# Kernel optimization log

Measured on AMD Instinct MI355X. Metric: run time of the kernel, lower is better.

## Reference

```python
import jax, jax.numpy as jnp
import numpy as np

N_NODES = 170000
N_EDGES = 1200000
IN_C, HID_C, OUT_C = 128, 128, 40
BN_EPS = 1e-5


def setup_inputs() -> dict:
    key = jax.random.key(0)
    ks = jax.random.split(key, 12)
    def glorot(k, fan_in, fan_out):
        lim = (6.0 / (fan_in + fan_out)) ** 0.5
        return jax.random.uniform(k, (fan_in, fan_out), jnp.float32, -lim, lim)
    x = jax.random.normal(ks[0], (N_NODES, IN_C), jnp.float32)
    edge_index = jax.random.randint(ks[1], (2, N_EDGES), 0, N_NODES, jnp.int64)
    return {
        "x": x,
        "edge_index": edge_index,
        "W0": glorot(ks[2], IN_C, HID_C), "b0": jnp.zeros((HID_C,), jnp.float32),
        "g0": jnp.ones((HID_C,), jnp.float32), "be0": jnp.zeros((HID_C,), jnp.float32),
        "W1": glorot(ks[3], HID_C, HID_C), "b1": jnp.zeros((HID_C,), jnp.float32),
        "g1": jnp.ones((HID_C,), jnp.float32), "be1": jnp.zeros((HID_C,), jnp.float32),
        "W2": glorot(ks[4], HID_C, OUT_C), "b2": jnp.zeros((OUT_C,), jnp.float32),
    }


def _gcn_norm(edge_index, num_nodes):
    # add self-loops, symmetric normalization (PyG GCNConv default)
    loop = jnp.arange(num_nodes, dtype=edge_index.dtype)
    src = jnp.concatenate([edge_index[0], loop])
    dst = jnp.concatenate([edge_index[1], loop])
    deg = jax.ops.segment_sum(jnp.ones_like(dst, jnp.float32), dst, num_segments=num_nodes)
    dinv = jnp.where(deg > 0, jax.lax.rsqrt(deg), 0.0)
    norm = dinv[src] * dinv[dst]  # [E+N]
    return src, dst, norm


def _conv(h, W, b, src, dst, norm, num_nodes):
    h = h @ W                              # [N, out]
    msg = h[src] * norm[:, None]           # gather + scale, [E+N, out]
    out = jax.ops.segment_sum(msg, dst, num_segments=num_nodes)
    return out + b


def _bn_relu(h, g, be):
    mean = jnp.mean(h, axis=0)
    var = jnp.mean(jnp.square(h - mean), axis=0)  # biased, as torch BN training
    h = (h - mean) * jax.lax.rsqrt(var + BN_EPS) * g + be
    return jax.nn.relu(h)


def reference(x, edge_index, W0, b0, g0, be0, W1, b1, g1, be1, W2, b2):
    N = x.shape[0]
    src, dst, norm = _gcn_norm(edge_index, N)
    h = _bn_relu(_conv(x, W0, b0, src, dst, norm, N), g0, be0)
    h = _bn_relu(_conv(h, W1, b1, src, dst, norm, N), g1, be1)
    return _conv(h, W2, b2, src, dst, norm, N)
```

## Files before the change

kernel.cpp:

```cpp
#include <hip/hip_runtime.h>

#define BN_EPS 1e-5f
#define CAP 3072

using bf16x8 = __attribute__((ext_vector_type(8))) short;
using f32x4  = __attribute__((ext_vector_type(4))) float;

__device__ __forceinline__ unsigned int f2bf(float f) {
    unsigned int u = __float_as_uint(f);
    u += 0x7fffu + ((u >> 16) & 1u);
    return u >> 16;
}
__device__ __forceinline__ unsigned int f2bf2(float lo, float hi) {
    unsigned int r;
    asm("v_cvt_pk_bf16_f32 %0, %1, %2" : "=v"(r) : "v"(lo), "v"(hi));
    return r;
}
__device__ __forceinline__ float bflo(unsigned int u) { return __uint_as_float(u << 16); }
__device__ __forceinline__ float bfhi(unsigned int u) { return __uint_as_float(u & 0xffff0000u); }

__global__ __launch_bounds__(256) void k_bscatter(const int* __restrict__ ei,
                                                  int* __restrict__ bcur,
                                                  unsigned int* __restrict__ ebuf,
                                                  int E, int NB) {
    __shared__ int h[768];
    __shared__ int wb[768];
    for (int i = threadIdx.x; i < 768; i += 256) h[i] = 0;
    __syncthreads();
    int base = blockIdx.x * 8192;
    int rk[32];
    #pragma unroll
    for (int it = 0; it < 32; ++it) {
        int e = base + it * 256 + threadIdx.x;
        rk[it] = (e < E) ? atomicAdd(&h[ei[E + e] >> 8], 1) : 0;
    }
    __syncthreads();
    for (int i = threadIdx.x; i < NB; i += 256) {
        int c = h[i];
        wb[i] = c ? atomicAdd(&bcur[i], c) : 0;
    }
    __syncthreads();
    #pragma unroll
    for (int it = 0; it < 32; ++it) {
        int e = base + it * 256 + threadIdx.x;
        if (e < E) {
            unsigned s = (unsigned)ei[e], d = (unsigned)ei[E + e];
            int bk = (int)(d >> 8);
            int pos = wb[bk] + rk[it];
            if (pos < (bk + 1) * CAP)
                ebuf[pos] = s | ((d & 255u) << 24);
        }
    }
}

__global__ __launch_bounds__(256) void k_bfinal(const unsigned int* __restrict__ ebuf,
                                                const int* __restrict__ bcur,
                                                int* __restrict__ csr,
                                                int* __restrict__ rs,
                                                int* __restrict__ re,
                                                float* __restrict__ dinv, int N) {
    __shared__ int cnt[256];
    __shared__ int scn[256];
    __shared__ int cur[256];
    const int t = threadIdx.x, b = blockIdx.x;
    const int beg = b * CAP;
    const int cntE = min(bcur[b] - beg, CAP);
    cnt[t] = 0;
    __syncthreads();
    for (int j = t; j < cntE; j += 256)
        atomicAdd(&cnt[ebuf[beg + j] >> 24], 1);
    __syncthreads();
    int v = cnt[t];
    scn[t] = v;
    __syncthreads();
    for (int off = 1; off < 256; off <<= 1) {
        int x = (t >= off) ? scn[t - off] : 0;
        __syncthreads();
        scn[t] += x;
        __syncthreads();
    }
    int excl = scn[t] - v;
    int node = b * 256 + t;
    if (node < N) {
        rs[node]   = beg + excl;
        re[node]   = beg + excl + v;
        dinv[node] = rsqrtf((float)(1 + v));
    }
    cur[t] = beg + excl;
    __syncthreads();
    for (int j = t; j < cntE; j += 256) {
        unsigned e = ebuf[beg + j];
        int pos = atomicAdd(&cur[e >> 24], 1);
        csr[pos] = (int)(e & 0x00FFFFFFu);
    }
}

__global__ __launch_bounds__(256) void k_prepW3(const float* __restrict__ W0,
                                                const float* __restrict__ W1,
                                                const float* __restrict__ W2,
                                                unsigned short* __restrict__ Wf,
                                                int* __restrict__ bcur,
                                                float* __restrict__ stats, int NB) {
    int t = blockIdx.x * 256 + threadIdx.x;
    if (t < NB) bcur[t] = t * CAP;
    if (t < 512) stats[t] = 0.f;
    int wid = t >> 11;
    int f = t & 2047;
    const float* W = (wid == 0) ? W0 : (wid == 1) ? W1 : W2;
    int C = (wid == 2) ? 40 : 128;
    int lane = f & 63, frag = f >> 6;
    int kt = frag & 3, ct = frag >> 2;
    int r = lane & 15, q = lane >> 4;
    int col = ct * 16 + r;
    int kbase = kt * 32 + q * 8;
    unsigned int v[8];
    #pragma unroll
    for (int j = 0; j < 8; ++j)
        v[j] = (col < C) ? f2bf(W[(size_t)(kbase + j) * C + col]) : 0u;
    uint4 o;
    o.x = v[0] | (v[1] << 16);
    o.y = v[2] | (v[3] << 16);
    o.z = v[4] | (v[5] << 16);
    o.w = v[6] | (v[7] << 16);
    ((uint4*)Wf)[t] = o;
}

template <int NOCT, int OST>
__global__ __launch_bounds__(256) void k_gemm_mfma(
        const void* __restrict__ X, int xf32, const unsigned short* __restrict__ Wf,
        unsigned short* __restrict__ H, int N,
        const float* __restrict__ stats, const float* __restrict__ g,
        const float* __restrict__ be) {
    __shared__ unsigned short bF[NOCT * 4 * 512];
    __shared__ float2 bnss[128];
    const int tid = threadIdx.x;
    const int rowbase = blockIdx.x * 64;

    if (stats && tid < 128) {
        const float invN = 1.0f / (float)N;
        float mean = stats[tid] * invN;
        float var  = fmaf(-mean, mean, stats[128 + tid] * invN);
        float sc   = g[tid] * rsqrtf(var + BN_EPS);
        bnss[tid]  = make_float2(sc, fmaf(-mean, sc, be[tid]));
    }
    {
        const uint4* src = (const uint4*)Wf;
        uint4* dst = (uint4*)bF;
        #pragma unroll
        for (int i = 0; i < NOCT; ++i) dst[tid + 256 * i] = src[tid + 256 * i];
    }
    __syncthreads();

    const int wave = tid >> 6, lane = tid & 63;
    const int r = lane & 15, q = lane >> 4;
    const int row  = rowbase + wave * 16 + r;
    const int rowc = min(row, N - 1);

    bf16x8 afr[4];
    #pragma unroll
    for (int kt = 0; kt < 4; ++kt) {
        const int kc = kt * 32 + q * 8;
        float vv[8];
        if (xf32) {
            const float4* xp = (const float4*)((const float*)X + (size_t)rowc * 128 + kc);
            float4 p0 = xp[0], p1 = xp[1];
            vv[0] = p0.x; vv[1] = p0.y; vv[2] = p0.z; vv[3] = p0.w;
            vv[4] = p1.x; vv[5] = p1.y; vv[6] = p1.z; vv[7] = p1.w;
        } else {
            uint4 p = *((const uint4*)((const unsigned short*)X + (size_t)rowc * 128 + kc));
            vv[0] = bflo(p.x); vv[1] = bfhi(p.x);
            vv[2] = bflo(p.y); vv[3] = bfhi(p.y);
            vv[4] = bflo(p.z); vv[5] = bfhi(p.z);
            vv[6] = bflo(p.w); vv[7] = bfhi(p.w);
        }
        if (stats) {
            #pragma unroll
            for (int j = 0; j < 8; ++j) {
                float2 ss = bnss[kc + j];
                vv[j] = fmaxf(fmaf(vv[j], ss.x, ss.y), 0.0f);
            }
        }
        union { unsigned int u[4]; bf16x8 v; } pk;
        pk.u[0] = f2bf2(vv[0], vv[1]);
        pk.u[1] = f2bf2(vv[2], vv[3]);
        pk.u[2] = f2bf2(vv[4], vv[5]);
        pk.u[3] = f2bf2(vv[6], vv[7]);
        afr[kt] = pk.v;
    }

    f32x4 acc[NOCT];
    #pragma unroll
    for (int ct = 0; ct < NOCT; ++ct) acc[ct] = (f32x4){0.f, 0.f, 0.f, 0.f};

    #pragma unroll
    for (int kt = 0; kt < 4; ++kt) {
        #pragma unroll
        for (int ct = 0; ct < NOCT; ++ct) {
            bf16x8 b = ((const bf16x8*)bF)[(ct * 4 + kt) * 64 + lane];
            acc[ct] = __builtin_amdgcn_mfma_f32_16x16x32_bf16(afr[kt], b, acc[ct], 0, 0, 0);
        }
    }

    #pragma unroll
    for (int ct = 0; ct < NOCT; ++ct) {
        #pragma unroll
        for (int i = 0; i < 4; i += 2) {
            int row0 = rowbase + wave * 16 + q * 4 + i;
            unsigned int pk = f2bf2(acc[ct][i], acc[ct][i + 1]);
            if (row0 < N)
                H[(size_t)row0 * OST + ct * 16 + r] = (unsigned short)pk;
            if (row0 + 1 < N)
                H[(size_t)(row0 + 1) * OST + ct * 16 + r] = (unsigned short)(pk >> 16);
        }
    }
}

__global__ __launch_bounds__(256) void k_agg128(
        const unsigned short* __restrict__ H, const int* __restrict__ rs,
        const int* __restrict__ re, const int* __restrict__ csr,
        const float* __restrict__ dinv, const float* __restrict__ b,
        unsigned short* __restrict__ outb, int N) {
    int lane = threadIdx.x & 15;
    int node = blockIdx.x * 16 + (threadIdx.x >> 4);
    if (node >= N) return;
    float dd  = dinv[node];
    int   beg = rs[node];
    int   end = re[node];
    uint4 hp  = ((const uint4*)(H + (size_t)node * 128))[lane];
    float4 bb0 = ((const float4*)b)[lane * 2];
    float4 bb1 = ((const float4*)b)[lane * 2 + 1];
    float sl = dd * dd;
    float a0 = fmaf(bflo(hp.x), sl, bb0.x), a1 = fmaf(bfhi(hp.x), sl, bb0.y);
    float a2 = fmaf(bflo(hp.y), sl, bb0.z), a3 = fmaf(bfhi(hp.y), sl, bb0.w);
    float a4 = fmaf(bflo(hp.z), sl, bb1.x), a5 = fmaf(bfhi(hp.z), sl, bb1.y);
    float a6 = fmaf(bflo(hp.w), sl, bb1.z), a7 = fmaf(bfhi(hp.w), sl, bb1.w);
    int j = beg;
    for (; j + 2 <= end; j += 2) {
        int s0 = csr[j], s1 = csr[j + 1];
        float n0 = dinv[s0] * dd, n1 = dinv[s1] * dd;
        uint4 v0 = ((const uint4*)(H + (size_t)s0 * 128))[lane];
        uint4 v1 = ((const uint4*)(H + (size_t)s1 * 128))[lane];
        a0 = fmaf(bflo(v0.x), n0, fmaf(bflo(v1.x), n1, a0));
        a1 = fmaf(bfhi(v0.x), n0, fmaf(bfhi(v1.x), n1, a1));
        a2 = fmaf(bflo(v0.y), n0, fmaf(bflo(v1.y), n1, a2));
        a3 = fmaf(bfhi(v0.y), n0, fmaf(bfhi(v1.y), n1, a3));
        a4 = fmaf(bflo(v0.z), n0, fmaf(bflo(v1.z), n1, a4));
        a5 = fmaf(bfhi(v0.z), n0, fmaf(bfhi(v1.z), n1, a5));
        a6 = fmaf(bflo(v0.w), n0, fmaf(bflo(v1.w), n1, a6));
        a7 = fmaf(bfhi(v0.w), n0, fmaf(bfhi(v1.w), n1, a7));
    }
    if (j < end) {
        int s0 = csr[j];
        float n0 = dinv[s0] * dd;
        uint4 v0 = ((const uint4*)(H + (size_t)s0 * 128))[lane];
        a0 = fmaf(bflo(v0.x), n0, a0); a1 = fmaf(bfhi(v0.x), n0, a1);
        a2 = fmaf(bflo(v0.y), n0, a2); a3 = fmaf(bfhi(v0.y), n0, a3);
        a4 = fmaf(bflo(v0.z), n0, a4); a5 = fmaf(bfhi(v0.z), n0, a5);
        a6 = fmaf(bflo(v0.w), n0, a6); a7 = fmaf(bfhi(v0.w), n0, a7);
    }
    uint4 o;
    o.x = f2bf2(a0, a1);
    o.y = f2bf2(a2, a3);
    o.z = f2bf2(a4, a5);
    o.w = f2bf2(a6, a7);
    ((uint4*)(outb + (size_t)node * 128))[lane] = o;
}

__global__ __launch_bounds__(256) void k_agg40(
        const unsigned short* __restrict__ H, const int* __restrict__ rs,
        const int* __restrict__ re, const int* __restrict__ csr,
        const float* __restrict__ dinv, const float* __restrict__ b,
        float* __restrict__ out, int N) {
    int lane = threadIdx.x & 15;
    int node = blockIdx.x * 16 + (threadIdx.x >> 4);
    if (node >= N || lane >= 10) return;
    float dd  = dinv[node];
    int   beg = rs[node];
    int   end = re[node];
    uint2 hp  = ((const uint2*)(H + (size_t)node * 64))[lane];
    float4 bb = ((const float4*)b)[lane];
    float  sl = dd * dd;
    float4 acc = make_float4(fmaf(bflo(hp.x), sl, bb.x), fmaf(bfhi(hp.x), sl, bb.y),
                             fmaf(bflo(hp.y), sl, bb.z), fmaf(bfhi(hp.y), sl, bb.w));
    int j = beg;
    for (; j + 2 <= end; j += 2) {
        int s0 = csr[j], s1 = csr[j + 1];
        float n0 = dinv[s0] * dd, n1 = dinv[s1] * dd;
        uint2 v0 = ((const uint2*)(H + (size_t)s0 * 64))[lane];
        uint2 v1 = ((const uint2*)(H + (size_t)s1 * 64))[lane];
        acc.x = fmaf(bflo(v0.x), n0, fmaf(bflo(v1.x), n1, acc.x));
        acc.y = fmaf(bfhi(v0.x), n0, fmaf(bfhi(v1.x), n1, acc.y));
        acc.z = fmaf(bflo(v0.y), n0, fmaf(bflo(v1.y), n1, acc.z));
        acc.w = fmaf(bfhi(v0.y), n0, fmaf(bfhi(v1.y), n1, acc.w));
    }
    if (j < end) {
        int s0 = csr[j];
        float n0 = dinv[s0] * dd;
        uint2 v0 = ((const uint2*)(H + (size_t)s0 * 64))[lane];
        acc.x = fmaf(bflo(v0.x), n0, acc.x);
        acc.y = fmaf(bfhi(v0.x), n0, acc.y);
        acc.z = fmaf(bflo(v0.y), n0, acc.z);
        acc.w = fmaf(bfhi(v0.y), n0, acc.w);
    }
    ((float4*)(out + (size_t)node * 40))[lane] = acc;
}

__global__ __launch_bounds__(256) void k_bnstats(
        const unsigned short* __restrict__ Bb, float* __restrict__ stats, int N) {
    __shared__ float red[2][16][128];
    const int t = threadIdx.x;
    const int lane16 = t & 15, grp = t >> 4;
    const int cbase = lane16 * 8;
    float s[8], q[8];
    #pragma unroll
    for (int k = 0; k < 8; ++k) { s[k] = 0.f; q[k] = 0.f; }

    const int step = gridDim.x * 16;
    for (int r = blockIdx.x * 16 + grp; r < N; r += 2 * step) {
        uint4 p0 = *((const uint4*)(Bb + (size_t)r * 128 + cbase));
        int r1 = r + step;
        if (r1 < N) {
            uint4 p1 = *((const uint4*)(Bb + (size_t)r1 * 128 + cbase));
            float v[8] = {bflo(p1.x), bfhi(p1.x), bflo(p1.y), bfhi(p1.y),
                          bflo(p1.z), bfhi(p1.z), bflo(p1.w), bfhi(p1.w)};
            #pragma unroll
            for (int k = 0; k < 8; ++k) { s[k] += v[k]; q[k] = fmaf(v[k], v[k], q[k]); }
        }
        float u[8] = {bflo(p0.x), bfhi(p0.x), bflo(p0.y), bfhi(p0.y),
                      bflo(p0.z), bfhi(p0.z), bflo(p0.w), bfhi(p0.w)};
        #pragma unroll
        for (int k = 0; k < 8; ++k) { s[k] += u[k]; q[k] = fmaf(u[k], u[k], q[k]); }
    }
    #pragma unroll
    for (int k = 0; k < 8; ++k) {
        red[0][grp][cbase + k] = s[k];
        red[1][grp][cbase + k] = q[k];
    }
    __syncthreads();
    if (t < 128) {
        float acc = 0.f;
        #pragma unroll
        for (int g = 0; g < 16; ++g) acc += red[0][g][t];
        unsafeAtomicAdd(&stats[t], acc);
    } else {
        int c = t - 128;
        float acc = 0.f;
        #pragma unroll
        for (int g = 0; g < 16; ++g) acc += red[1][g][c];
        unsafeAtomicAdd(&stats[128 + c], acc);
    }
}

extern "C" void kernel_launch(void* const* d_in, const int* in_sizes, int n_in,
                              void* d_out, int out_size, void* d_ws, size_t ws_size,
                              hipStream_t stream) {
    const float* x   = (const float*)d_in[0];
    const int*   ei  = (const int*)d_in[1];
    const float* W0  = (const float*)d_in[2];
    const float* b0  = (const float*)d_in[3];
    const float* g0  = (const float*)d_in[4];
    const float* be0 = (const float*)d_in[5];
    const float* W1  = (const float*)d_in[6];
    const float* b1  = (const float*)d_in[7];
    const float* g1  = (const float*)d_in[8];
    const float* be1 = (const float*)d_in[9];
    const float* W2  = (const float*)d_in[10];
    const float* b2  = (const float*)d_in[11];
    float* out = (float*)d_out;

    const int N  = in_sizes[0] / 128;
    const int E  = in_sizes[1] / 2;
    const int NB = (N + 255) >> 8;
    const int EB = (E + 8191) / 8192;

    float* ws   = (float*)d_ws;
    size_t Npad = ((size_t)N + 511) & ~(size_t)511;
    size_t BCAP = (size_t)NB * CAP;
    float* dinv = ws;
    int*   rs   = (int*)(ws + Npad);
    int*   re   = rs + Npad;
    int*   csr  = re + Npad;
    unsigned int* ebuf = (unsigned int*)(csr + BCAP);
    int*   bcur = (int*)(ebuf + BCAP);
    float* stats0 = (float*)(bcur + 1024);
    float* stats1 = stats0 + 256;
    unsigned short* Wf = (unsigned short*)(stats1 + 256);
    unsigned short* Hb = Wf + 3 * 16384;
    unsigned short* Bb = Hb + Npad * 128;

    k_prepW3  <<<24, 256, 0, stream>>>(W0, W1, W2, Wf, bcur, stats0, NB);
    k_bscatter<<<EB, 256, 0, stream>>>(ei, bcur, ebuf, E, NB);
    k_bfinal  <<<NB, 256, 0, stream>>>(ebuf, bcur, csr, rs, re, dinv, N);

    int gemm_grid = (N + 63) / 64;
    int agg_grid  = (N + 15) / 16;

    k_gemm_mfma<8, 128><<<gemm_grid, 256, 0, stream>>>(x, 1, Wf, Hb, N,
                                                       nullptr, nullptr, nullptr);
    k_agg128<<<agg_grid, 256, 0, stream>>>(Hb, rs, re, csr, dinv, b0, Bb, N);
    k_bnstats<<<512, 256, 0, stream>>>(Bb, stats0, N);

    k_gemm_mfma<8, 128><<<gemm_grid, 256, 0, stream>>>(Bb, 0, Wf + 16384, Hb, N,
                                                       stats0, g0, be0);
    k_agg128<<<agg_grid, 256, 0, stream>>>(Hb, rs, re, csr, dinv, b1, Bb, N);
    k_bnstats<<<512, 256, 0, stream>>>(Bb, stats1, N);

    k_gemm_mfma<3, 64><<<gemm_grid, 256, 0, stream>>>(Bb, 0, Wf + 2 * 16384, Hb, N,
                                                      stats1, g1, be1);
    k_agg40<<<agg_grid, 256, 0, stream>>>(Hb, rs, re, csr, dinv, b2, out, N);
}
```

Measured before the change: 455.4 us.

## Fuse BN-ReLU, aggregation and GEMM by aggregating before the transform

Layers 2 and 3 now compute (A·relu(bn(h)))·W instead of A·(relu(bn(h))·W). One fused kernel applies BN+ReLU to each gathered neighbor row, aggregates all 128 channels, stages the 16-node tile in LDS, and multiplies it by W with MFMA before writing the result. This removes two standalone GEMM kernels and their intermediate write and reread. The cost is that the last layer now gathers 128-wide rows instead of 40-wide ones, BN is recomputed for every edge, and the bf16 output is written with scattered 2-byte stores.

```diff
diff --git a/kernel.cpp b/kernel.cpp
--- a/kernel.cpp
+++ b/kernel.cpp
@@ -266,43 +266,127 @@
     ((uint4*)(outb + (size_t)node * 128))[lane] = o;
 }
 
-__global__ __launch_bounds__(256) void k_agg40(
-        const unsigned short* __restrict__ H, const int* __restrict__ rs,
+#define BNACC8(v, n)                                                   \
+    a0 = fmaf(fmaxf(fmaf(bflo(v.x), sc0, sh0), 0.f), n, a0);           \
+    a1 = fmaf(fmaxf(fmaf(bfhi(v.x), sc1, sh1), 0.f), n, a1);           \
+    a2 = fmaf(fmaxf(fmaf(bflo(v.y), sc2, sh2), 0.f), n, a2);           \
+    a3 = fmaf(fmaxf(fmaf(bfhi(v.y), sc3, sh3), 0.f), n, a3);           \
+    a4 = fmaf(fmaxf(fmaf(bflo(v.z), sc4, sh4), 0.f), n, a4);           \
+    a5 = fmaf(fmaxf(fmaf(bfhi(v.z), sc5, sh5), 0.f), n, a5);           \
+    a6 = fmaf(fmaxf(fmaf(bflo(v.w), sc6, sh6), 0.f), n, a6);           \
+    a7 = fmaf(fmaxf(fmaf(bfhi(v.w), sc7, sh7), 0.f), n, a7);
+
+template <int NOCT, bool F32OUT>
+__global__ __launch_bounds__(256) void k_fused_ag(
+        const unsigned short* __restrict__ Hin, const int* __restrict__ rs,
         const int* __restrict__ re, const int* __restrict__ csr,
-        const float* __restrict__ dinv, const float* __restrict__ b,
-        float* __restrict__ out, int N) {
-    int lane = threadIdx.x & 15;
-    int node = blockIdx.x * 16 + (threadIdx.x >> 4);
-    if (node >= N || lane >= 10) return;
-    float dd  = dinv[node];
-    int   beg = rs[node];
-    int   end = re[node];
-    uint2 hp  = ((const uint2*)(H + (size_t)node * 64))[lane];
-    float4 bb = ((const float4*)b)[lane];
-    float  sl = dd * dd;
-    float4 acc = make_float4(fmaf(bflo(hp.x), sl, bb.x), fmaf(bfhi(hp.x), sl, bb.y),
-                             fmaf(bflo(hp.y), sl, bb.z), fmaf(bfhi(hp.y), sl, bb.w));
+        const float* __restrict__ dinv,
+        const float* __restrict__ stats, const float* __restrict__ g,
+        const float* __restrict__ be,
+        const unsigned short* __restrict__ Wfrag, const float* __restrict__ bias,
+        void* __restrict__ outp, int N) {
+    __shared__ unsigned short A[16][136];
+    const int t = threadIdx.x;
+    const int lane16 = t & 15, grp = t >> 4;
+    const int node = blockIdx.x * 16 + grp;
+    const int cbase = lane16 * 8;
+    const float invN = 1.0f / (float)N;
+
+    float sc0, sc1, sc2, sc3, sc4, sc5, sc6, sc7;
+    float sh0, sh1, sh2, sh3, sh4, sh5, sh6, sh7;
+    {
+        float scv[8], shv[8];
+        #pragma unroll
+        for (int k = 0; k < 8; ++k) {
+            float mean = stats[cbase + k] * invN;
+            float var  = fmaf(-mean, mean, stats[128 + cbase + k] * invN);
+            float s    = g[cbase + k] * rsqrtf(var + BN_EPS);
+            scv[k] = s; shv[k] = fmaf(-mean, s, be[cbase + k]);
+        }
+        sc0 = scv[0]; sc1 = scv[1]; sc2 = scv[2]; sc3 = scv[3];
+        sc4 = scv[4]; sc5 = scv[5]; sc6 = scv[6]; sc7 = scv[7];
+        sh0 = shv[0]; sh1 = shv[1]; sh2 = shv[2]; sh3 = shv[3];
+        sh4 = shv[4]; sh5 = shv[5]; sh6 = shv[6]; sh7 = shv[7];
+    }
+
+    const bool valid = node < N;
+    const int  nodec = valid ? node : 0;
+    float dd  = valid ? dinv[nodec] : 0.f;
+    int   beg = valid ? rs[nodec] : 0;
+    int   end = valid ? re[nodec] : 0;
+    uint4 hp  = ((const uint4*)(Hin + (size_t)nodec * 128))[lane16];
+    float sl  = dd * dd;
+    float a0 = 0.f, a1 = 0.f, a2 = 0.f, a3 = 0.f;
+    float a4 = 0.f, a5 = 0.f, a6 = 0.f, a7 = 0.f;
+    BNACC8(hp, sl);
     int j = beg;
     for (; j + 2 <= end; j += 2) {
         int s0 = csr[j], s1 = csr[j + 1];
         float n0 = dinv[s0] * dd, n1 = dinv[s1] * dd;
-        uint2 v0 = ((const uint2*)(H + (size_t)s0 * 64))[lane];
-        uint2 v1 = ((const uint2*)(H + (size_t)s1 * 64))[lane];
-        acc.x = fmaf(bflo(v0.x), n0, fmaf(bflo(v1.x), n1, acc.x));
-        acc.y = fmaf(bfhi(v0.x), n0, fmaf(bfhi(v1.x), n1, acc.y));
-        acc.z = fmaf(bflo(v0.y), n0, fmaf(bflo(v1.y), n1, acc.z));
-        acc.w = fmaf(bfhi(v0.y), n0, fmaf(bfhi(v1.y), n1, acc.w));
+        uint4 v0 = ((const uint4*)(Hin + (size_t)s0 * 128))[lane16];
+        uint4 v1 = ((const uint4*)(Hin + (size_t)s1 * 128))[lane16];
+        BNACC8(v0, n0);
+        BNACC8(v1, n1);
     }
     if (j < end) {
         int s0 = csr[j];
         float n0 = dinv[s0] * dd;
-        uint2 v0 = ((const uint2*)(H + (size_t)s0 * 64))[lane];
-        acc.x = fmaf(bflo(v0.x), n0, acc.x);
-        acc.y = fmaf(bfhi(v0.x), n0, acc.y);
-        acc.z = fmaf(bflo(v0.y), n0, acc.z);
-        acc.w = fmaf(bfhi(v0.y), n0, acc.w);
-    }
-    ((float4*)(out + (size_t)node * 40))[lane] = acc;
+        uint4 v0 = ((const uint4*)(Hin + (size_t)s0 * 128))[lane16];
+        BNACC8(v0, n0);
+    }
+
+    uint4 o;
+    o.x = f2bf2(a0, a1);
+    o.y = f2bf2(a2, a3);
+    o.z = f2bf2(a4, a5);
+    o.w = f2bf2(a6, a7);
+    *((uint4*)&A[grp][lane16 * 8]) = o;
+    __syncthreads();
+
+    const int wave = t >> 6, lane = t & 63;
+    const int col = lane & 15, q = lane >> 4;
+    bf16x8 afr[4];
+    #pragma unroll
+    for (int kt = 0; kt < 4; ++kt)
+        afr[kt] = *((const bf16x8*)&A[col][kt * 32 + q * 8]);
+
+    constexpr int CPW = (NOCT + 3) / 4;
+    #pragma unroll
+    for (int c = 0; c < CPW; ++c) {
+        const int ct = wave + 4 * c;
+        if (ct < NOCT) {
+            f32x4 acc = (f32x4){0.f, 0.f, 0.f, 0.f};
+            #pragma unroll
+            for (int kt = 0; kt < 4; ++kt) {
+                bf16x8 b = ((const bf16x8*)Wfrag)[(ct * 4 + kt) * 64 + lane];
+                acc = __builtin_amdgcn_mfma_f32_16x16x32_bf16(afr[kt], b, acc, 0, 0, 0);
+            }
+            if (F32OUT) {
+                const int ch = ct * 16 + col;
+                if (ch < 40) {
+                    float bv = bias[ch];
+                    float* out = (float*)outp;
+                    #pragma unroll
+                    for (int i = 0; i < 4; ++i) {
+                        int r0 = blockIdx.x * 16 + q * 4 + i;
+                        if (r0 < N) out[(size_t)r0 * 40 + ch] = acc[i] + bv;
+                    }
+                }
+            } else {
+                float bv = bias[ct * 16 + col];
+                unsigned short* H2 = (unsigned short*)outp;
+                #pragma unroll
+                for (int i = 0; i < 4; i += 2) {
+                    int r0 = blockIdx.x * 16 + q * 4 + i;
+                    unsigned int pk = f2bf2(acc[i] + bv, acc[i + 1] + bv);
+                    if (r0 < N)
+                        H2[(size_t)r0 * 128 + ct * 16 + col] = (unsigned short)pk;
+                    if (r0 + 1 < N)
+                        H2[(size_t)(r0 + 1) * 128 + ct * 16 + col] = (unsigned short)(pk >> 16);
+                }
+            }
+        }
+    }
 }
 
 __global__ __launch_bounds__(256) void k_bnstats(
@@ -400,12 +484,12 @@
     k_agg128<<<agg_grid, 256, 0, stream>>>(Hb, rs, re, csr, dinv, b0, Bb, N);
     k_bnstats<<<512, 256, 0, stream>>>(Bb, stats0, N);
 
-    k_gemm_mfma<8, 128><<<gemm_grid, 256, 0, stream>>>(Bb, 0, Wf + 16384, Hb, N,
-                                                       stats0, g0, be0);
-    k_agg128<<<agg_grid, 256, 0, stream>>>(Hb, rs, re, csr, dinv, b1, Bb, N);
-    k_bnstats<<<512, 256, 0, stream>>>(Bb, stats1, N);
-
-    k_gemm_mfma<3, 64><<<gemm_grid, 256, 0, stream>>>(Bb, 0, Wf + 2 * 16384, Hb, N,
-                                                      stats1, g1, be1);
-    k_agg40<<<agg_grid, 256, 0, stream>>>(Hb, rs, re, csr, dinv, b2, out, N);
-}
+    k_fused_ag<8, false><<<agg_grid, 256, 0, stream>>>(Bb, rs, re, csr, dinv,
+                                                       stats0, g0, be0,
+                                                       Wf + 16384, b1, Hb, N);
+    k_bnstats<<<512, 256, 0, stream>>>(Hb, stats1, N);
+
+    k_fused_ag<3, true><<<agg_grid, 256, 0, stream>>>(Hb, rs, re, csr, dinv,
+                                                      stats1, g1, be1,
+                                                      Wf + 2 * 16384, b2, out, N);
+}
```

Result: no change. 458.6 us (+0.7%).
